# Kernel tuning notes

Measured on AMD Instinct MI355X. Metric: run time of the kernel, lower is better.

Reference implementation:

```python
import jax, jax.numpy as jnp
import numpy as np

N, T = 8, 64
V = [2048, 1024, 512, 256, 128]
E = [12288, 6144, 3072, 1536, 768]
NF = [1, 8, 16, 32, 64, 128]
LAT, INIT_DIM = 64, 16
K3 = 27  # 3x3x3 spline kernel bank


def setup_inputs():
    ks = iter(jax.random.split(jax.random.key(0), 80))
    inp = {}
    inp['x'] = jax.random.normal(next(ks), (N, V[0], T), jnp.float32)
    for l in range(5):
        inp['edge_index%d' % l] = jax.random.randint(next(ks), (2, E[l]), 0, V[l])
        inp['edge_attr%d' % l] = jax.random.uniform(next(ks), (E[l], 3), jnp.float32)
    pools = {'P01': (V[1], V[0]), 'P12': (V[2], V[1]), 'P23': (V[3], V[2]), 'P34': (V[4], V[3]),
             'P43': (V[3], V[4]), 'P32': (V[2], V[3]), 'P21': (V[1], V[2]), 'P10': (V[0], V[1])}
    for n, sh in pools.items():
        inp[n] = jax.random.normal(next(ks), sh, jnp.float32) / np.float32(np.sqrt(sh[1]))
    convs = {'conv1_w': (NF[0], NF[1]), 'conv2_w': (NF[1], NF[2]), 'conv3_w': (NF[2], NF[3]), 'conv4_w': (NF[3], NF[4]),
             'deconv4_w': (NF[4], NF[3]), 'deconv3_w': (NF[3], NF[2]), 'deconv2_w': (NF[2], NF[1]), 'deconv1_w': (NF[1], NF[0])}
    for n, (ci, co) in convs.items():
        inp[n] = jax.random.normal(next(ks), (K3, ci, co), jnp.float32) / np.float32(np.sqrt(ci * 8))
    def lin(k, o, i):
        return jax.random.normal(k, (o, i), jnp.float32) / np.float32(np.sqrt(i))
    inp['fce1_w'] = lin(next(ks), NF[5], NF[4]); inp['fce1_b'] = jnp.zeros((NF[5],), jnp.float32)
    inp['fce2_w'] = lin(next(ks), LAT, NF[5]); inp['fce2_b'] = jnp.zeros((LAT,), jnp.float32)
    inp['fcd3_w'] = lin(next(ks), NF[5], LAT); inp['fcd3_b'] = jnp.zeros((NF[5],), jnp.float32)
    inp['fcd4_w'] = lin(next(ks), NF[4], NF[5]); inp['fcd4_b'] = jnp.zeros((NF[4],), jnp.float32)
    for pre in ('dom', 'ini'):
        inp[pre + '_Wih'] = lin(next(ks), 3 * LAT, LAT)
        inp[pre + '_Whh'] = lin(next(ks), 3 * LAT, LAT)
        inp[pre + '_bih'] = jnp.zeros((3 * LAT,), jnp.float32)
        inp[pre + '_bhh'] = jnp.zeros((3 * LAT,), jnp.float32)
        inp[pre + '_agg_w'] = lin(next(ks), LAT, LAT)
        inp[pre + '_agg_b'] = jnp.zeros((LAT,), jnp.float32)
    for g in ('r', 'u', 'c'):
        inp['tr_W' + g] = lin(next(ks), LAT, 2 * LAT)
        inp['tr_b' + g] = jnp.zeros((LAT,), jnp.float32)
    return inp


def _edge_weights(attr, W):
    # Degree-1 B-spline basis over 3-dim pseudo-coords, kernel_size=3 per dim.
    pos = attr * 2.0                                    # [0, ks-1]
    i0 = jnp.clip(jnp.floor(pos), 0.0, 1.0).astype(jnp.int32)
    f = pos - i0                                        # fractional part
    We = jnp.zeros((attr.shape[0], W.shape[1], W.shape[2]), W.dtype)
    for c0 in (0, 1):
        w0 = f[:, 0] if c0 else 1.0 - f[:, 0]
        for c1 in (0, 1):
            w1 = f[:, 1] if c1 else 1.0 - f[:, 1]
            for c2 in (0, 1):
                w2 = f[:, 2] if c2 else 1.0 - f[:, 2]
                flat = (i0[:, 0] + c0) * 9 + (i0[:, 1] + c1) * 3 + (i0[:, 2] + c2)
                We = We + (w0 * w1 * w2)[:, None, None] * W[flat]
    return We                                           # (E, Ci, Co)


def _spatial_block(x, edge_index, edge_attr, W):
    # x: (N, V, Ci, T); edge-conditioned graph conv per time step, mean-aggregated, ELU.
    Nn, Vv, Ci, Tt = x.shape
    We = _edge_weights(edge_attr, W)                    # (E, Ci, Co)
    src, dst = edge_index[0], edge_index[1]
    msg = jnp.einsum('neit,eio->enot', x[:, src], We)   # (E, N, Co, T)
    agg = jax.ops.segment_sum(msg, dst, num_segments=Vv)
    deg = jax.ops.segment_sum(jnp.ones((dst.shape[0],), x.dtype), dst, num_segments=Vv)
    agg = agg / jnp.maximum(deg, 1.0)[:, None, None, None]
    return jax.nn.elu(agg.transpose(1, 0, 2, 3))        # (N, V, Co, T)


def _pw(x, Wl, b):
    # 1x1 Conv2d over channel dim: x (N, V, C, T)
    return jnp.einsum('nvct,oc->nvot', x, Wl) + b[None, None, :, None]


def _pool(h, P):
    # torch.matmul(P, x.view(N, V, C*T))
    Nn, Vv, Cc, Tt = h.shape
    return jnp.matmul(P, h.reshape(Nn, Vv, Cc * Tt)).reshape(Nn, P.shape[0], Cc, Tt)


def _rnn_encode(x, Wih, Whh, bih, bhh):
    # GRU over time per node; x (N, V, C, T) -> hidden seq (N, V, H, T)
    Nn, Vv, Cc, Tt = x.shape
    xt = x.transpose(3, 0, 1, 2).reshape(Tt, Nn * Vv, Cc)
    H = Whh.shape[1]
    def step(h, xi):
        gi = xi @ Wih.T + bih
        gh = h @ Whh.T + bhh
        ir, iz, ig = jnp.split(gi, 3, axis=-1)
        hr, hz, hg = jnp.split(gh, 3, axis=-1)
        r = jax.nn.sigmoid(ir + hr)
        z = jax.nn.sigmoid(iz + hz)
        g = jnp.tanh(ig + r * hg)
        hn = (1.0 - z) * g + z * h
        return hn, hn
    h0 = jnp.zeros((Nn * Vv, H), x.dtype)
    _, hs = jax.lax.scan(step, h0, xt)
    return hs.reshape(Tt, Nn, Vv, H).transpose(1, 2, 3, 0)


def reference(x, edge_attr0, edge_attr1, edge_attr2, edge_attr3, edge_attr4, P01, P12, P23, P34, P43, P32, P21, P10, conv1_w, conv2_w, conv3_w, conv4_w, deconv4_w, deconv3_w, deconv2_w, deconv1_w, fce1_w, fce1_b, fce2_w, fce2_b, fcd3_w, fcd3_b, fcd4_w, fcd4_b, dom_Wih, dom_Whh, dom_bih, dom_bhh, dom_agg_w, dom_agg_b, ini_Wih, ini_Whh, ini_bih, ini_bhh, ini_agg_w, ini_agg_b, tr_Wr, tr_br, tr_Wu, tr_bu, tr_Wc, tr_bc, edge_index0, edge_index1, edge_index2, edge_index3, edge_index4):
    h = x.reshape(N, V[0], NF[0], T)
    h = _pool(_spatial_block(h, edge_index0, edge_attr0, conv1_w), P01)
    h = _pool(_spatial_block(h, edge_index1, edge_attr1, conv2_w), P12)
    h = _pool(_spatial_block(h, edge_index2, edge_attr2, conv3_w), P23)
    h = _pool(_spatial_block(h, edge_index3, edge_attr3, conv4_w), P34)
    h = jax.nn.elu(_pw(h, fce1_w, fce1_b))
    embed = jnp.tanh(_pw(h, fce2_w, fce2_b))            # (N, V4, LAT, T)
    # ---- latent domain + initial state ----
    dom = _rnn_encode(embed, dom_Wih, dom_Whh, dom_bih, dom_bhh)
    z_D = jnp.tanh(dom[..., -1] @ dom_agg_w.T + dom_agg_b)
    ini = _rnn_encode(embed[..., :INIT_DIM], ini_Wih, ini_Whh, ini_bih, ini_bhh)
    z_0 = jnp.tanh(ini[..., -1] @ ini_agg_w.T + ini_agg_b)
    # ---- recurrent latent propagation over T steps (gated transition) ----
    def step(zp, _):
        cat = jnp.concatenate([zp, z_D], axis=-1)
        r = jax.nn.sigmoid(cat @ tr_Wr.T + tr_br)
        u = jax.nn.sigmoid(cat @ tr_Wu.T + tr_bu)
        c = jnp.tanh(jnp.concatenate([r * zp, z_D], axis=-1) @ tr_Wc.T + tr_bc)
        zt = (1.0 - u) * zp + u * c
        return zt, zt
    _, zs = jax.lax.scan(step, z_0, None, length=T)
    z = zs.transpose(1, 2, 3, 0)                        # (N, V4, LAT, T)
    h = jax.nn.elu(_pw(z, fcd3_w, fcd3_b))
    h = jax.nn.elu(_pw(h, fcd4_w, fcd4_b))
    h = _spatial_block(_pool(h, P43), edge_index3, edge_attr3, deconv4_w)
    h = _spatial_block(_pool(h, P32), edge_index2, edge_attr2, deconv3_w)
    h = _spatial_block(_pool(h, P21), edge_index1, edge_attr1, deconv2_w)
    h = _spatial_block(_pool(h, P10), edge_index0, edge_attr0, deconv1_w)
    return h.reshape(N, V[0], T)
```

## Files before the change

### kernel.cpp

```cpp
#include <hip/hip_runtime.h>

#define NB 8
#define TT 64

typedef __attribute__((ext_vector_type(8))) short bf16x8_t;
typedef __attribute__((ext_vector_type(4))) float f32x4_t;

__device__ __forceinline__ float sigm(float x){ return 1.0f/(1.0f+expf(-x)); }
__device__ __forceinline__ float eluf(float x){ return x>0.0f ? x : expm1f(x); }
__device__ __forceinline__ ushort f2bf(float f){
  uint u = __float_as_uint(f);
  return (ushort)((u + 0x7FFFu + ((u >> 16) & 1u)) >> 16);
}
__device__ __forceinline__ float bf2f(ushort u){
  return __uint_as_float(((uint)u) << 16);
}

__device__ __constant__ int c_VL[4] = {2048, 1024, 512, 256};
__device__ __constant__ int c_VO[4] = {0, 2048, 3072, 3584};
__device__ __constant__ int c_EO[4] = {0, 12288, 18432, 21504};
#define TOTV 3840
#define TOTE 23040

__global__ void transpose_kernel(const float* __restrict__ in, float* __restrict__ out, int R, int C){
  int idx = blockIdx.x*256 + threadIdx.x;
  if (idx >= R*C) return;
  int r = idx / C, c = idx - r*C;
  out[c*R + r] = in[idx];
}

__global__ void conv_bf16(const float* __restrict__ in, ushort* __restrict__ out, int n){
  int i = blockIdx.x*256 + threadIdx.x;
  if (i < n) out[i] = f2bf(in[i]);
}

__global__ void pad_wih(const float* __restrict__ in, ushort* __restrict__ out){
  int i = blockIdx.x*256 + threadIdx.x;
  if (i >= 256*64) return;
  int r = i >> 6;
  out[i] = (r < 192) ? f2bf(in[i]) : (ushort)0;
}

__global__ __launch_bounds__(256) void transp_bf16(
    const float* __restrict__ in, ushort* __restrict__ out, int R, int Ccols){
  __shared__ float tile[64][65];
  int n = blockIdx.z;
  const float* ip = in + (size_t)n*R*Ccols;
  ushort* op = out + (size_t)n*R*Ccols;
  int tid = threadIdx.x;
  int tx = tid & 63, ty = tid >> 6;
  int r0 = blockIdx.y*64, c0 = blockIdx.x*64;
  #pragma unroll
  for (int i = 0; i < 64; i += 4)
    tile[ty+i][tx] = ip[(size_t)(r0+ty+i)*Ccols + c0 + tx];
  __syncthreads();
  #pragma unroll
  for (int i = 0; i < 64; i += 4)
    op[(size_t)(c0+ty+i)*R + r0 + tx] = f2bf(tile[tx][ty+i]);
}

template<int Ci, int CiP>
__global__ __launch_bounds__(256) void xpose_bf16(const float* __restrict__ in, ushort* __restrict__ out){
  __shared__ float tile[Ci][65];
  int s = blockIdx.x, tid = threadIdx.x;
  const float* ip = in + (size_t)s*Ci*64;
  for (int i = tid; i < Ci*64; i += 256) tile[i>>6][i&63] = ip[i];
  __syncthreads();
  ushort* op = out + (size_t)s*64*CiP;
  for (int i = tid; i < 64*CiP; i += 256){
    int t = i / CiP, ci = i - t*CiP;
    op[i] = (ci < Ci) ? f2bf(tile[ci][t]) : (ushort)0;
  }
}

__global__ void csr_zero(int* __restrict__ deg_all){
  int i = blockIdx.x*256 + threadIdx.x;
  if (i < TOTV) deg_all[i] = 0;
}

__global__ void csr_deg(const int* __restrict__ d0, const int* __restrict__ d1,
                        const int* __restrict__ d2, const int* __restrict__ d3,
                        int* __restrict__ deg_all){
  int idx = blockIdx.x*256 + threadIdx.x;
  if (idx >= TOTE) return;
  int l = (idx < 12288) ? 0 : (idx < 18432) ? 1 : (idx < 21504) ? 2 : 3;
  int e = idx - c_EO[l];
  const int* dl = (l==0)?d0:(l==1)?d1:(l==2)?d2:d3;
  atomicAdd(&deg_all[c_VO[l] + dl[e]], 1);
}

__global__ __launch_bounds__(1024) void csr_scan(const int* __restrict__ deg_all,
                                                 int* __restrict__ rowptr_all,
                                                 int* __restrict__ cursor_all){
  __shared__ int a[2048], b[2048];
  int l = blockIdx.x;
  int Vv = c_VL[l], vo = c_VO[l], eo = c_EO[l];
  int tid = threadIdx.x;
  for (int i = tid; i < 2048; i += 1024) a[i] = (i < Vv) ? deg_all[vo + i] : 0;
  __syncthreads();
  int* s = a; int* d = b;
  for (int off = 1; off < 2048; off <<= 1){
    for (int i = tid; i < 2048; i += 1024) d[i] = s[i] + ((i >= off) ? s[i-off] : 0);
    __syncthreads();
    int* t = s; s = d; d = t;
  }
  int rbase = vo + l;
  for (int i = tid; i < Vv; i += 1024){
    int excl = (i == 0) ? 0 : s[i-1];
    rowptr_all[rbase + i] = excl;
    cursor_all[vo + i]    = eo + excl;
  }
  if (tid == 0) rowptr_all[rbase + Vv] = s[2047];
}

__global__ void csr_fill(const int* __restrict__ d0, const int* __restrict__ d1,
                         const int* __restrict__ d2, const int* __restrict__ d3,
                         int* __restrict__ cursor_all, int* __restrict__ elist_all){
  int idx = blockIdx.x*256 + threadIdx.x;
  if (idx >= TOTE) return;
  int l = (idx < 12288) ? 0 : (idx < 18432) ? 1 : (idx < 21504) ? 2 : 3;
  int e = idx - c_EO[l];
  const int* dl = (l==0)?d0:(l==1)?d1:(l==2)?d2:d3;
  int p = atomicAdd(&cursor_all[c_VO[l] + dl[e]], 1);
  elist_all[p] = e;
}

__global__ void csr_sort(const int* __restrict__ rowptr_all, int* __restrict__ elist_all){
  int idx = blockIdx.x*256 + threadIdx.x;
  if (idx >= TOTV) return;
  int l = (idx < 2048) ? 0 : (idx < 3072) ? 1 : (idx < 3584) ? 2 : 3;
  int v = idx - c_VO[l];
  int rbase = c_VO[l] + l, eo = c_EO[l];
  int s = eo + rowptr_all[rbase + v], epos = eo + rowptr_all[rbase + v + 1];
  for (int i = s + 1; i < epos; ++i){
    int key = elist_all[i];
    int j = i - 1;
    while (j >= s && elist_all[j] > key){ elist_all[j+1] = elist_all[j]; --j; }
    elist_all[j+1] = key;
  }
}

__global__ void edge_we_kernel(const float* __restrict__ attr, const float* __restrict__ Wb,
                               float* __restrict__ We, int E, int CiCo){
  int idx = blockIdx.x*256 + threadIdx.x;
  if (idx >= E*CiCo) return;
  int e = idx / CiCo, r = idx - e*CiCo;
  float f[3]; int i0[3];
  #pragma unroll
  for (int d = 0; d < 3; ++d){
    float p  = attr[e*3+d]*2.0f;
    float fl = fminf(fmaxf(floorf(p), 0.0f), 1.0f);
    i0[d] = (int)fl;
    f[d]  = p - fl;
  }
  float acc = 0.0f;
  #pragma unroll
  for (int c0 = 0; c0 < 2; ++c0){
    float w0 = c0 ? f[0] : 1.0f - f[0];
    #pragma unroll
    for (int c1 = 0; c1 < 2; ++c1){
      float w1 = c1 ? f[1] : 1.0f - f[1];
      #pragma unroll
      for (int c2 = 0; c2 < 2; ++c2){
        float w2 = c2 ? f[2] : 1.0f - f[2];
        int flat = (i0[0]+c0)*9 + (i0[1]+c1)*3 + (i0[2]+c2);
        acc += w0*w1*w2 * Wb[flat*CiCo + r];
      }
    }
  }
  We[idx] = acc;
}

template<int Ci, int Co, int CiP>
__global__ __launch_bounds__(256) void edge_weT2(
    const float* __restrict__ attr, const float* __restrict__ Wb,
    ushort* __restrict__ WeT){
  __shared__ float s[Ci][Co + 1];
  int e = blockIdx.x, tid = threadIdx.x;
  float f[3]; int i0[3];
  #pragma unroll
  for (int d = 0; d < 3; ++d){
    float p  = attr[e*3+d]*2.0f;
    float fl = fminf(fmaxf(floorf(p), 0.0f), 1.0f);
    i0[d] = (int)fl;
    f[d]  = p - fl;
  }
  float w[8]; int fl8[8];
  #pragma unroll
  for (int c0 = 0; c0 < 2; ++c0)
    #pragma unroll
    for (int c1 = 0; c1 < 2; ++c1)
      #pragma unroll
      for (int c2 = 0; c2 < 2; ++c2){
        int k = c0*4 + c1*2 + c2;
        w[k] = (c0 ? f[0] : 1.0f - f[0]) * (c1 ? f[1] : 1.0f - f[1]) * (c2 ? f[2] : 1.0f - f[2]);
        fl8[k] = (i0[0]+c0)*9 + (i0[1]+c1)*3 + (i0[2]+c2);
      }
  constexpr int CiCo = Ci*Co;
  for (int r = tid; r < CiCo; r += 256){
    float acc = 0.0f;
    #pragma unroll
    for (int k = 0; k < 8; ++k) acc += w[k]*Wb[fl8[k]*CiCo + r];
    s[r/Co][r - (r/Co)*Co] = acc;
  }
  __syncthreads();
  ushort* op = WeT + (size_t)e*(Co*CiP);
  for (int r2 = tid; r2 < Co*CiP; r2 += 256){
    int co = r2 / CiP, ci = r2 - co*CiP;
    op[r2] = (ci < Ci) ? f2bf(s[ci][co]) : (ushort)0;
  }
}

template<int Ci, int Co>
__global__ __launch_bounds__(256) void gconv2_kernel(
    const float* __restrict__ x, const float* __restrict__ We,
    const int* __restrict__ src_arr, const int* __restrict__ rowptr,
    const int* __restrict__ elist, float* __restrict__ out, int V){
  constexpr int CiCo = Ci*Co;
  __shared__ float ws[4][CiCo];
  __shared__ float red[Co*64];
  int blk = blockIdx.x;
  int n = blk / V, v = blk - n*V;
  int tid = threadIdx.x;
  int w = tid >> 6, lane = tid & 63;
  int rs = rowptr[v], re = rowptr[v+1];
  float acc[Co];
  #pragma unroll
  for (int i = 0; i < Co; ++i) acc[i] = 0.0f;

  for (int q = rs + w; q < re; q += 4){
    int e   = elist[q];
    int src = src_arr[e];
    const float* wsrc = We + (size_t)e*CiCo;
    #pragma unroll
    for (int i = lane; i < CiCo; i += 64) ws[w][i] = wsrc[i];
    __builtin_amdgcn_s_waitcnt(0);
    const float* xp = x + ((size_t)(n*V + src))*(Ci*64) + lane;
    #pragma unroll 4
    for (int ci = 0; ci < Ci; ++ci){
      float xv = xp[(size_t)ci*64];
      if constexpr (Co >= 4){
        #pragma unroll
        for (int co = 0; co < Co; co += 4){
          float4 wv = *(const float4*)&ws[w][ci*Co + co];
          acc[co+0] += wv.x*xv;
          acc[co+1] += wv.y*xv;
          acc[co+2] += wv.z*xv;
          acc[co+3] += wv.w*xv;
        }
      } else {
        #pragma unroll
        for (int co = 0; co < Co; ++co) acc[co] += ws[w][ci*Co + co]*xv;
      }
    }
  }

  if (w == 0){
    #pragma unroll
    for (int co = 0; co < Co; ++co) red[co*64 + lane] = acc[co];
  }
  __syncthreads();
  #pragma unroll
  for (int ww = 1; ww < 4; ++ww){
    if (w == ww){
      #pragma unroll
      for (int co = 0; co < Co; ++co) red[co*64 + lane] += acc[co];
    }
    __syncthreads();
  }
  float scale = 1.0f / fmaxf((float)(re - rs), 1.0f);
  size_t ob = ((size_t)(n*V + v))*(Co*64);
  for (int co = w; co < Co; co += 4)
    out[ob + (size_t)co*64 + lane] = eluf(red[co*64 + lane]*scale);
}

template<int CiP, int Co>
__global__ __launch_bounds__(256, 4) void gconv_mfma4(
    const ushort* __restrict__ xT, const ushort* __restrict__ WeT,
    const int* __restrict__ src_arr, const int* __restrict__ rowptr,
    const int* __restrict__ elist, float* __restrict__ out, int V){
  constexpr int MT = Co/16, KT = CiP/32;
  __shared__ int2 es[64];
  __shared__ float red[Co*64];
  int blk = blockIdx.x;
  int n = blk / V, v = blk - n*V;
  int tid = threadIdx.x;
  int w = tid >> 6, lane = tid & 63;
  int l15 = lane & 15, g = lane >> 4;
  int rs = rowptr[v], re = rowptr[v+1];
  int deg = re - rs;
  int cnt0 = (deg < 64) ? deg : 64;
  if (tid < cnt0){
    int e = elist[rs + tid];
    es[tid] = make_int2(e, src_arr[e]);
  }
  __syncthreads();
  f32x4_t acc[MT][4];
  #pragma unroll
  for (int m = 0; m < MT; ++m)
    #pragma unroll
    for (int tt = 0; tt < 4; ++tt) acc[m][tt] = (f32x4_t){0.f,0.f,0.f,0.f};
  for (int q = w; q < deg; q += 4){
    int e, src;
    if (q < 64){ e = es[q].x; src = es[q].y; }
    else { e = elist[rs + q]; src = src_arr[e]; }
    const ushort* xp = xT + ((size_t)(n*V + src))*(64*CiP) + (size_t)l15*CiP + g*8;
    const ushort* wp = WeT + (size_t)e*(Co*CiP) + (size_t)l15*CiP + g*8;
    #pragma unroll
    for (int kt = 0; kt < KT; ++kt){
      bf16x8_t bfrag[4];
      #pragma unroll
      for (int tt = 0; tt < 4; ++tt)
        bfrag[tt] = *(const bf16x8_t*)(xp + (size_t)tt*16*CiP + kt*32);
      #pragma unroll
      for (int m = 0; m < MT; ++m){
        bf16x8_t afrag = *(const bf16x8_t*)(wp + (size_t)m*16*CiP + kt*32);
        #pragma unroll
        for (int tt = 0; tt < 4; ++tt)
          acc[m][tt] = __builtin_amdgcn_mfma_f32_16x16x32_bf16(afrag, bfrag[tt], acc[m][tt], 0, 0, 0);
      }
    }
  }
  if (w == 0){
    #pragma unroll
    for (int m = 0; m < MT; ++m)
      #pragma unroll
      for (int tt = 0; tt < 4; ++tt)
        #pragma unroll
        for (int r = 0; r < 4; ++r)
          red[(m*16 + g*4 + r)*64 + tt*16 + l15] = acc[m][tt][r];
  }
  __syncthreads();
  #pragma unroll
  for (int ww = 1; ww < 4; ++ww){
    if (w == ww){
      #pragma unroll
      for (int m = 0; m < MT; ++m)
        #pragma unroll
        for (int tt = 0; tt < 4; ++tt)
          #pragma unroll
          for (int r = 0; r < 4; ++r)
            red[(m*16 + g*4 + r)*64 + tt*16 + l15] += acc[m][tt][r];
    }
    __syncthreads();
  }
  float scale = 1.0f / fmaxf((float)deg, 1.0f);
  size_t ob = ((size_t)(n*V + v))*(Co*64);
  for (int i = tid; i < Co*64; i += 256)
    out[ob + i] = eluf(red[i]*scale);
}

template<int OUTBF>
__global__ __launch_bounds__(256) void pool_mfma64(
    const ushort* __restrict__ A, const ushort* __restrict__ BT, void* __restrict__ Cout,
    int M, int K, int NN){
  __shared__ ushort As[64*40];
  __shared__ ushort Bs[64*40];
  char* Asb = (char*)As; char* Bsb = (char*)Bs;
  int tid = threadIdx.x;
  int wv = tid >> 6, lane = tid & 63;
  int g = lane >> 4, l15 = lane & 15;
  int wr = wv >> 1, wc = wv & 1;
  int m0 = blockIdx.y*64, n0 = blockIdx.x*64;
  const ushort* Bp = BT + (size_t)blockIdx.z*((size_t)NN*K);
  f32x4_t acc[2][2];
  #pragma unroll
  for (int i = 0; i < 2; ++i)
    #pragma unroll
    for (int j = 0; j < 2; ++j) acc[i][j] = (f32x4_t){0.f,0.f,0.f,0.f};
  int srow = tid >> 2, slot = tid & 3;
  int wbo = srow*80 + slot*16;
  const ushort* gA = A  + (size_t)(m0+srow)*K + slot*8;
  const ushort* gB = Bp + (size_t)(n0+srow)*K + slot*8;
  for (int k0 = 0; k0 < K; k0 += 32){
    uint4 va = *(const uint4*)(gA + k0);
    uint4 vb = *(const uint4*)(gB + k0);
    __syncthreads();
    *(uint4*)(Asb + wbo) = va;
    *(uint4*)(Bsb + wbo) = vb;
    __syncthreads();
    bf16x8_t af[2], bfr[2];
    #pragma unroll
    for (int f = 0; f < 2; ++f){
      af[f]  = *(const bf16x8_t*)(Asb + (wr*32 + f*16 + l15)*80 + g*16);
      bfr[f] = *(const bf16x8_t*)(Bsb + (wc*32 + f*16 + l15)*80 + g*16);
    }
    #pragma unroll
    for (int fm = 0; fm < 2; ++fm)
      #pragma unroll
      for (int fn = 0; fn < 2; ++fn)
        acc[fm][fn] = __builtin_amdgcn_mfma_f32_16x16x32_bf16(af[fm], bfr[fn], acc[fm][fn], 0, 0, 0);
  }
  #pragma unroll
  for (int fm = 0; fm < 2; ++fm){
    int row = m0 + wr*32 + fm*16 + g*4;
    #pragma unroll
    for (int fn = 0; fn < 2; ++fn){
      int col = n0 + wc*32 + fn*16 + l15;
      if constexpr (OUTBF){
        ushort* Cb = (ushort*)Cout + (size_t)blockIdx.z*((size_t)M*NN);
        #pragma unroll
        for (int r = 0; r < 4; ++r)
          Cb[(size_t)(row + r)*NN + col] = f2bf(acc[fm][fn][r]);
      } else {
        float* Cf = (float*)Cout + (size_t)blockIdx.z*((size_t)M*NN);
        #pragma unroll
        for (int r = 0; r < 4; ++r)
          Cf[(size_t)(row + r)*NN + col] = acc[fm][fn][r];
      }
    }
  }
}

template<int C, int O1, int O2, int ACT1, int ACT2, int INF, int OUTF>
__global__ __launch_bounds__(256) void pw2_mfma(
    const void* __restrict__ inv,
    const ushort* __restrict__ W1, const float* __restrict__ b1,
    const ushort* __restrict__ W2, const float* __restrict__ b2,
    void* __restrict__ outv){
  constexpr int CP = C + 8, O1P = O1 + 8;
  constexpr int MT1 = O1/16, KT1 = C/32;
  constexpr int MT2 = O2/16, KT2 = O1/32;
  __shared__ ushort XT[64*CP];
  __shared__ ushort YT[64*O1P];
  int s = blockIdx.x, tid = threadIdx.x;
  int w = tid >> 6, lane = tid & 63;
  int l15 = lane & 15, g = lane >> 4;
  if constexpr (INF == 0){
    const float* ip = (const float*)inv + (size_t)s*C*64;
    for (int i = tid; i < C*64; i += 256){ int c = i >> 6, t = i & 63; XT[t*CP + c] = f2bf(ip[i]); }
  } else {
    const float* ip = (const float*)inv + (size_t)s*64*C;
    for (int i = tid; i < C*64; i += 256){ int t = i / C, c = i - t*C; XT[t*CP + c] = f2bf(ip[i]); }
  }
  __syncthreads();
  int trow = w*16 + l15;
  {
    f32x4_t acc[MT1];
    #pragma unroll
    for (int m = 0; m < MT1; ++m) acc[m] = (f32x4_t){0.f,0.f,0.f,0.f};
    #pragma unroll
    for (int kt = 0; kt < KT1; ++kt){
      bf16x8_t bfrag = *(const bf16x8_t*)(&XT[trow*CP + kt*32 + g*8]);
      #pragma unroll
      for (int m = 0; m < MT1; ++m){
        bf16x8_t afrag = *(const bf16x8_t*)(W1 + (size_t)(m*16 + l15)*C + kt*32 + g*8);
        acc[m] = __builtin_amdgcn_mfma_f32_16x16x32_bf16(afrag, bfrag, acc[m], 0, 0, 0);
      }
    }
    #pragma unroll
    for (int m = 0; m < MT1; ++m){
      #pragma unroll
      for (int r = 0; r < 4; ++r){
        int o = m*16 + g*4 + r;
        float v = acc[m][r] + b1[o];
        v = (ACT1 == 1) ? eluf(v) : tanhf(v);
        YT[trow*O1P + o] = f2bf(v);
      }
    }
  }
  __syncthreads();
  {
    f32x4_t acc[MT2];
    #pragma unroll
    for (int m = 0; m < MT2; ++m) acc[m] = (f32x4_t){0.f,0.f,0.f,0.f};
    #pragma unroll
    for (int kt = 0; kt < KT2; ++kt){
      bf16x8_t bfrag = *(const bf16x8_t*)(&YT[trow*O1P + kt*32 + g*8]);
      #pragma unroll
      for (int m = 0; m < MT2; ++m){
        bf16x8_t afrag = *(const bf16x8_t*)(W2 + (size_t)(m*16 + l15)*O1 + kt*32 + g*8);
        acc[m] = __builtin_amdgcn_mfma_f32_16x16x32_bf16(afrag, bfrag, acc[m], 0, 0, 0);
      }
    }
    if constexpr (OUTF == 0){
      float* op = (float*)outv + (size_t)s*O2*64;
      #pragma unroll
      for (int m = 0; m < MT2; ++m){
        #pragma unroll
        for (int r = 0; r < 4; ++r){
          int o = m*16 + g*4 + r;
          float v = acc[m][r] + b2[o];
          v = (ACT2 == 1) ? eluf(v) : tanhf(v);
          op[(size_t)o*64 + trow] = v;
        }
      }
    } else {
      constexpr int O2P = O2 + 8;
      #pragma unroll
      for (int m = 0; m < MT2; ++m){
        #pragma unroll
        for (int r = 0; r < 4; ++r){
          int o = m*16 + g*4 + r;
          float v = acc[m][r] + b2[o];
          v = (ACT2 == 1) ? eluf(v) : tanhf(v);
          XT[trow*O2P + o] = f2bf(v);
        }
      }
      __syncthreads();
      ushort* op = (ushort*)outv + (size_t)s*64*O2;
      for (int i = tid; i < 64*O2; i += 256){
        int t = i / O2, o = i - t*O2;
        op[i] = XT[t*O2P + o];
      }
    }
  }
}

__global__ __launch_bounds__(192) void gru3m_kernel(
    const ushort* __restrict__ GI_d, const ushort* __restrict__ GI_i,
    const float* __restrict__ WhhT_d, const float* __restrict__ WhhT_i,
    const float* __restrict__ bih_d, const float* __restrict__ bhh_d,
    const float* __restrict__ aggT_d, const float* __restrict__ aggb_d,
    const float* __restrict__ bih_i, const float* __restrict__ bhh_i,
    const float* __restrict__ aggT_i, const float* __restrict__ aggb_i,
    float* __restrict__ zD, float* __restrict__ z0, int S){
  __shared__ float hsh[64];
  __shared__ float rbuf[64];
  __shared__ float zbuf[64];
  int bid = blockIdx.x;
  bool dom = (bid < S);
  int s = dom ? bid : bid - S;
  int TS = dom ? 64 : 16;
  const ushort* GI   = dom ? GI_d   : GI_i;
  const float* WhhT  = dom ? WhhT_d : WhhT_i;
  const float* bih   = dom ? bih_d  : bih_i;
  const float* bhh   = dom ? bhh_d  : bhh_i;
  const float* aggT  = dom ? aggT_d : aggT_i;
  const float* aggb  = dom ? aggb_d : aggb_i;
  float* zout        = dom ? zD     : z0;
  int tid = threadIdx.x;
  int g = tid >> 6, j = tid & 63;
  if (tid < 64) hsh[tid] = 0.0f;
  float whh[64];
  #pragma unroll
  for (int c = 0; c < 64; ++c) whh[c] = WhhT[c*192 + tid];
  float b_i = bih[tid], b_h = bhh[tid];
  const ushort* gp = GI + (size_t)s*64*256 + tid;
  float gi_cur = b_i + bf2f(gp[0]);
  __syncthreads();
  for (int t = 0; t < TS; ++t){
    ushort gnx = (t + 1 < TS) ? gp[(size_t)(t+1)*256] : (ushort)0;
    float gh0 = 0.f, gh1 = 0.f;
    #pragma unroll
    for (int c4 = 0; c4 < 16; ++c4){
      float4 hv = *(const float4*)&hsh[c4*4];
      gh0 += whh[c4*4+0]*hv.x; gh1 += whh[c4*4+1]*hv.y;
      gh0 += whh[c4*4+2]*hv.z; gh1 += whh[c4*4+3]*hv.w;
    }
    float gh = b_h + gh0 + gh1;
    if (g == 0)      rbuf[j] = sigm(gi_cur + gh);
    else if (g == 1) zbuf[j] = sigm(gi_cur + gh);
    __syncthreads();
    if (g == 2){
      float gg = tanhf(gi_cur + rbuf[j]*gh);
      float z  = zbuf[j];
      hsh[j] = (1.0f - z)*gg + z*hsh[j];
    }
    __syncthreads();
    gi_cur = b_i + bf2f(gnx);
  }
  if (tid < 64){
    float a = aggb[tid];
    #pragma unroll
    for (int c = 0; c < 64; ++c) a += aggT[c*64 + tid]*hsh[c];
    zout[(size_t)s*64 + tid] = tanhf(a);
  }
}

__global__ __launch_bounds__(192) void trans2_kernel(
    const float* __restrict__ z0, const float* __restrict__ zD,
    const float* __restrict__ WrT, const float* __restrict__ WuT, const float* __restrict__ WcT,
    const float* __restrict__ br, const float* __restrict__ bu, const float* __restrict__ bc,
    float* __restrict__ zs){
  __shared__ float zp[64];
  __shared__ float zd[64];
  __shared__ float rz[64];
  __shared__ float ubuf[64];
  int s = blockIdx.x, tid = threadIdx.x;
  int g = tid >> 6, j = tid & 63;
  if (tid < 64){ zp[tid] = z0[(size_t)s*64 + tid]; zd[tid] = zD[(size_t)s*64 + tid]; }
  const float* WT = (g == 0) ? WrT : (g == 1) ? WuT : WcT;
  const float* bb = (g == 0) ? br  : (g == 1) ? bu  : bc;
  float wv[64];
  #pragma unroll
  for (int c = 0; c < 64; ++c) wv[c] = WT[c*64 + j];
  float bconst = bb[j];
  __syncthreads();
  {
    float a0 = 0.f, a1 = 0.f;
    #pragma unroll
    for (int c4 = 0; c4 < 16; ++c4){
      float4 dv = *(const float4*)&zd[c4*4];
      a0 += WT[(64 + c4*4 + 0)*64 + j]*dv.x;
      a1 += WT[(64 + c4*4 + 1)*64 + j]*dv.y;
      a0 += WT[(64 + c4*4 + 2)*64 + j]*dv.z;
      a1 += WT[(64 + c4*4 + 3)*64 + j]*dv.w;
    }
    bconst += a0 + a1;
  }
  for (int t = 0; t < 64; ++t){
    if (g < 2){
      float a0 = 0.f, a1 = 0.f;
      #pragma unroll
      for (int c4 = 0; c4 < 16; ++c4){
        float4 pv = *(const float4*)&zp[c4*4];
        a0 += wv[c4*4+0]*pv.x; a1 += wv[c4*4+1]*pv.y;
        a0 += wv[c4*4+2]*pv.z; a1 += wv[c4*4+3]*pv.w;
      }
      float v = sigm(bconst + a0 + a1);
      if (g == 0) rz[j]   = v*zp[j];
      else        ubuf[j] = v;
    }
    __syncthreads();
    if (g == 2){
      float a0 = 0.f, a1 = 0.f;
      #pragma unroll
      for (int c4 = 0; c4 < 16; ++c4){
        float4 rv = *(const float4*)&rz[c4*4];
        a0 += wv[c4*4+0]*rv.x; a1 += wv[c4*4+1]*rv.y;
        a0 += wv[c4*4+2]*rv.z; a1 += wv[c4*4+3]*rv.w;
      }
      float cc = tanhf(bconst + a0 + a1);
      float u  = ubuf[j];
      float zt = (1.0f - u)*zp[j] + u*cc;
      zs[(size_t)s*4096 + t*64 + j] = zt;
      zp[j] = zt;
    }
    __syncthreads();
  }
}

extern "C" void kernel_launch(void* const* d_in, const int* in_sizes, int n_in,
                              void* d_out, int out_size, void* d_ws, size_t ws_size,
                              hipStream_t stream){
  static const int Vl[5] = {2048, 1024, 512, 256, 128};
  static const int El[5] = {12288, 6144, 3072, 1536, 768};
  static const int VO[4] = {0, 2048, 3072, 3584};
  static const int EO[4] = {0, 12288, 18432, 21504};

  const float* xin = (const float*)d_in[0];
  const int*   ei[4]; const float* ea[4];
  for (int l = 0; l < 4; ++l){ ei[l] = (const int*)d_in[1 + 2*l]; ea[l] = (const float*)d_in[2 + 2*l]; }
  const float* Psrc[8] = {(const float*)d_in[11], (const float*)d_in[12], (const float*)d_in[13], (const float*)d_in[14],
                          (const float*)d_in[15], (const float*)d_in[16], (const float*)d_in[17], (const float*)d_in[18]};
  const float* conv_w[4]   = {(const float*)d_in[19], (const float*)d_in[20], (const float*)d_in[21], (const float*)d_in[22]};
  const float* deconv_w[4] = {(const float*)d_in[23], (const float*)d_in[24], (const float*)d_in[25], (const float*)d_in[26]};
  const float* fce1_w = (const float*)d_in[27]; const float* fce1_b = (const float*)d_in[28];
  const float* fce2_w = (const float*)d_in[29]; const float* fce2_b = (const float*)d_in[30];
  const float* fcd3_w = (const float*)d_in[31]; const float* fcd3_b = (const float*)d_in[32];
  const float* fcd4_w = (const float*)d_in[33]; const float* fcd4_b = (const float*)d_in[34];
  const float* dom_Wih = (const float*)d_in[35]; const float* dom_Whh = (const float*)d_in[36];
  const float* dom_bih = (const float*)d_in[37]; const float* dom_bhh = (const float*)d_in[38];
  const float* dom_aggw = (const float*)d_in[39]; const float* dom_aggb = (const float*)d_in[40];
  const float* ini_Wih = (const float*)d_in[41]; const float* ini_Whh = (const float*)d_in[42];
  const float* ini_bih = (const float*)d_in[43]; const float* ini_bhh = (const float*)d_in[44];
  const float* ini_aggw = (const float*)d_in[45]; const float* ini_aggb = (const float*)d_in[46];
  const float* tr_Wr = (const float*)d_in[47]; const float* tr_br = (const float*)d_in[48];
  const float* tr_Wu = (const float*)d_in[49]; const float* tr_bu = (const float*)d_in[50];
  const float* tr_Wc = (const float*)d_in[51]; const float* tr_bc = (const float*)d_in[52];

  char* wsp = (char*)d_ws;
  size_t off = 0;
  auto carve = [&](size_t bytes) -> void* {
    void* p = wsp + off;
    off = (off + bytes + 255) & ~(size_t)255;
    return p;
  };
  const size_t BUFCAP = (size_t)NB*2048*8*64;
  float* bufA = (float*)carve(BUFCAP*4);
  float* bufB = (float*)carve(BUFCAP*4);
  void* webt = carve((size_t)NB*1024*1024*2 + 1024);
  float*  We = (float*)webt;
  ushort* BT = (ushort*)webt;
  ushort* xT = (ushort*)webt;
  ushort* WeTb = (ushort*)carve((size_t)1536*64*32*2 + 1024);
  ushort* embB2 = (ushort*)carve((size_t)1024*64*64*2);
  float* zD   = (float*)carve((size_t)NB*128*64*4);
  float* z0   = (float*)carve((size_t)NB*128*64*4);
  float* domWhhT = (float*)carve(12288*4);
  float* iniWhhT = (float*)carve(12288*4);
  float* domAggT = (float*)carve(4096*4);
  float* iniAggT = (float*)carve(4096*4);
  float* trWrT   = (float*)carve(8192*4);
  float* trWuT   = (float*)carve(8192*4);
  float* trWcT   = (float*)carve(8192*4);
  ushort* WihPadD = (ushort*)carve(256*64*2);
  ushort* WihPadI = (ushort*)carve(256*64*2);
  ushort* Wfce1b = (ushort*)carve(8192*2);
  ushort* Wfce2b = (ushort*)carve(8192*2);
  ushort* Wfcd3b = (ushort*)carve(8192*2);
  ushort* Wfcd4b = (ushort*)carve(8192*2);
  static const int PM[8] = {1024, 512, 256, 128, 256, 512, 1024, 2048};
  static const int PK[8] = {2048, 1024, 512, 256, 128, 256, 512, 1024};
  ushort* Pb[8];
  for (int i = 0; i < 8; ++i) Pb[i] = (ushort*)carve((size_t)PM[i]*PK[i]*2);
  int* deg_all    = (int*)carve(TOTV*4);
  int* cursor_all = (int*)carve(TOTV*4);
  int* rowptr_all = (int*)carve((TOTV + 4)*4);
  int* elist_all  = (int*)carve(TOTE*4);
  (void)ws_size; (void)in_sizes; (void)n_in; (void)out_size;

  auto tr = [&](const float* in, float* out, int R, int C){
    transpose_kernel<<<(R*C + 255)/256, 256, 0, stream>>>(in, out, R, C);
  };
  tr(dom_Whh, domWhhT, 192, 64);  tr(ini_Whh, iniWhhT, 192, 64);
  tr(dom_aggw, domAggT, 64, 64);  tr(ini_aggw, iniAggT, 64, 64);
  tr(tr_Wr, trWrT, 64, 128);  tr(tr_Wu, trWuT, 64, 128);  tr(tr_Wc, trWcT, 64, 128);
  pad_wih<<<64, 256, 0, stream>>>(dom_Wih, WihPadD);
  pad_wih<<<64, 256, 0, stream>>>(ini_Wih, WihPadI);
  conv_bf16<<<32, 256, 0, stream>>>(fce1_w, Wfce1b, 8192);
  conv_bf16<<<32, 256, 0, stream>>>(fce2_w, Wfce2b, 8192);
  conv_bf16<<<32, 256, 0, stream>>>(fcd3_w, Wfcd3b, 8192);
  conv_bf16<<<32, 256, 0, stream>>>(fcd4_w, Wfcd4b, 8192);
  for (int i = 0; i < 8; ++i){
    int nel = PM[i]*PK[i];
    conv_bf16<<<(nel + 255)/256, 256, 0, stream>>>(Psrc[i], Pb[i], nel);
  }

  const int* dsts[4] = {ei[0] + El[0], ei[1] + El[1], ei[2] + El[2], ei[3] + El[3]};
  csr_zero<<<(TOTV + 255)/256, 256, 0, stream>>>(deg_all);
  csr_deg <<<(TOTE + 255)/256, 256, 0, stream>>>(dsts[0], dsts[1], dsts[2], dsts[3], deg_all);
  csr_scan<<<4, 1024, 0, stream>>>(deg_all, rowptr_all, cursor_all);
  csr_fill<<<(TOTE + 255)/256, 256, 0, stream>>>(dsts[0], dsts[1], dsts[2], dsts[3], cursor_all, elist_all);
  csr_sort<<<(TOTV + 255)/256, 256, 0, stream>>>(rowptr_all, elist_all);

  auto gconv = [&](const float* in, float* out, int l, const float* Wb, int Ci, int Co){
    int CiCo = Ci*Co;
    int tot = El[l]*CiCo;
    edge_we_kernel<<<(tot + 255)/256, 256, 0, stream>>>(ea[l], Wb, We, El[l], CiCo);
    int nblk = NB*Vl[l];
    const int* rp = rowptr_all + VO[l] + l;
    const int* el = elist_all + EO[l];
    #define GCASE(CI,CO) if (Ci==CI && Co==CO) gconv2_kernel<CI,CO><<<nblk, 256, 0, stream>>>(in, We, ei[l], rp, el, out, Vl[l]);
    GCASE(1,8)  GCASE(8,16)  GCASE(16,8)  GCASE(8,1)
    #undef GCASE
  };
  auto gconv_m = [&](const float* in, float* out, int l, const float* Wb, int Ci, int Co){
    int S = NB*Vl[l];
    int CiP = (Ci < 32) ? 32 : Ci;
    if (Ci == 16)      xpose_bf16<16,32><<<S, 256, 0, stream>>>(in, xT);
    else if (Ci == 32) xpose_bf16<32,32><<<S, 256, 0, stream>>>(in, xT);
    else               xpose_bf16<64,64><<<S, 256, 0, stream>>>(in, xT);
    if (Ci == 16 && Co == 32)      edge_weT2<16,32,32><<<El[l], 256, 0, stream>>>(ea[l], Wb, WeTb);
    else if (Ci == 32 && Co == 64) edge_weT2<32,64,32><<<El[l], 256, 0, stream>>>(ea[l], Wb, WeTb);
    else if (Ci == 64 && Co == 32) edge_weT2<64,32,64><<<El[l], 256, 0, stream>>>(ea[l], Wb, WeTb);
    else if (Ci == 32 && Co == 16) edge_weT2<32,16,32><<<El[l], 256, 0, stream>>>(ea[l], Wb, WeTb);
    const int* rp = rowptr_all + VO[l] + l;
    const int* el = elist_all + EO[l];
    #define GMC(CIP,CO) if (CiP==CIP && Co==CO) gconv_mfma4<CIP,CO><<<S, 256, 0, stream>>>(xT, WeTb, ei[l], rp, el, out, Vl[l]);
    GMC(32,32) GMC(32,64) GMC(64,32) GMC(32,16)
    #undef GMC
  };
  auto pool2 = [&](int pi, const float* hin, float* out, int M, int K, int NN){
    dim3 tg(NN/64, K/64, NB);
    transp_bf16<<<tg, 256, 0, stream>>>(hin, BT, K, NN);
    dim3 g(NN/64, M/64, NB);
    pool_mfma64<0><<<g, 256, 0, stream>>>(Pb[pi], BT, (void*)out, M, K, NN);
  };

  gconv(xin,  bufA, 0, conv_w[0], 1, 8);
  pool2(0, bufA, bufB, 1024, 2048, 512);
  gconv(bufB, bufA, 1, conv_w[1], 8, 16);
  pool2(1, bufA, bufB, 512, 1024, 1024);
  gconv_m(bufB, bufA, 2, conv_w[2], 16, 32);
  pool2(2, bufA, bufB, 256, 512, 2048);
  gconv_m(bufB, bufA, 3, conv_w[3], 32, 64);
  pool2(3, bufA, bufB, 128, 256, 4096);

  pw2_mfma<64,128,64,1,2,0,1><<<1024, 256, 0, stream>>>(bufB, Wfce1b, fce1_b, Wfce2b, fce2_b, embB2);

  dim3 gg(4, 1024, 1);
  pool_mfma64<1><<<gg, 256, 0, stream>>>(embB2, WihPadD, (void*)bufA, 65536, 64, 256);
  pool_mfma64<1><<<gg, 256, 0, stream>>>(embB2, WihPadI, (void*)bufB, 65536, 64, 256);
  gru3m_kernel<<<2*NB*128, 192, 0, stream>>>((const ushort*)bufA, (const ushort*)bufB,
      domWhhT, iniWhhT, dom_bih, dom_bhh, domAggT, dom_aggb,
      ini_bih, ini_bhh, iniAggT, ini_aggb, zD, z0, NB*128);
  trans2_kernel<<<NB*128, 192, 0, stream>>>(z0, zD, trWrT, trWuT, trWcT, tr_br, tr_bu, tr_bc, bufA);

  pw2_mfma<64,128,64,1,1,1,0><<<1024, 256, 0, stream>>>(bufA, Wfcd3b, fcd3_b, Wfcd4b, fcd4_b, bufB);
  pool2(4, bufB, bufA, 256, 128, 4096);
  gconv_m(bufA, bufB, 3, deconv_w[0], 64, 32);
  pool2(5, bufB, bufA, 512, 256, 2048);
  gconv_m(bufA, bufB, 2, deconv_w[1], 32, 16);
  pool2(6, bufB, bufA, 1024, 512, 1024);
  gconv(bufA, bufB, 1, deconv_w[2], 16, 8);
  pool2(7, bufB, bufA, 2048, 1024, 512);
  gconv(bufA, (float*)d_out, 0, deconv_w[3], 8, 1);
}
```

Measured before the change: 808.9 us.

## Batch weight-prep launches, merge input-gate GEMMs, and reorder gconv block mapping

Replaces about twenty small weight transpose and bf16-conversion launches with a single task-table kernel, which cuts launch overhead. The two GRU input-projection GEMMs become one GEMM against a concatenated 512-wide weight, and the GRU kernel reads the interleaved output with a 512 stride. The MFMA graph-conv kernel also remaps block IDs so consecutive blocks cover all batches of a node group, aiming for better cache reuse of shared edge weights. The remap assumes V is a multiple of 8 and NB equals 8.

```diff
diff --git a/kernel.cpp b/kernel.cpp
--- a/kernel.cpp
+++ b/kernel.cpp
@@ -22,23 +22,34 @@
 #define TOTV 3840
 #define TOTE 23040
 
-__global__ void transpose_kernel(const float* __restrict__ in, float* __restrict__ out, int R, int C){
-  int idx = blockIdx.x*256 + threadIdx.x;
-  if (idx >= R*C) return;
-  int r = idx / C, c = idx - r*C;
-  out[c*R + r] = in[idx];
-}
-
-__global__ void conv_bf16(const float* __restrict__ in, ushort* __restrict__ out, int n){
-  int i = blockIdx.x*256 + threadIdx.x;
-  if (i < n) out[i] = f2bf(in[i]);
-}
-
-__global__ void pad_wih(const float* __restrict__ in, ushort* __restrict__ out){
-  int i = blockIdx.x*256 + threadIdx.x;
-  if (i >= 256*64) return;
-  int r = i >> 6;
-  out[i] = (r < 192) ? f2bf(in[i]) : (ushort)0;
+#define NPREP 21
+struct PrepTasks {
+  const float* src[NPREP];
+  void* dst[NPREP];
+  int R[NPREP], C[NPREP];
+  int type[NPREP];
+  int blk0[NPREP + 1];
+  int ntask;
+};
+
+__global__ __launch_bounds__(256) void prep_all(PrepTasks T){
+  int b = blockIdx.x;
+  int t = 0;
+  while (t + 1 < T.ntask && b >= T.blk0[t+1]) ++t;
+  int idx = (b - T.blk0[t])*256 + threadIdx.x;
+  int n = T.R[t]*T.C[t];
+  if (idx >= n) return;
+  int ty = T.type[t];
+  if (ty == 0){
+    int C = T.C[t];
+    int r = idx / C, c = idx - r*C;
+    ((float*)T.dst[t])[c*T.R[t] + r] = T.src[t][idx];
+  } else if (ty == 1){
+    int r = idx >> 6;
+    ((ushort*)T.dst[t])[idx] = (r < 192) ? f2bf(T.src[t][idx]) : (ushort)0;
+  } else {
+    ((ushort*)T.dst[t])[idx] = f2bf(T.src[t][idx]);
+  }
 }
 
 __global__ __launch_bounds__(256) void transp_bf16(
@@ -282,8 +293,10 @@
   constexpr int MT = Co/16, KT = CiP/32;
   __shared__ int2 es[64];
   __shared__ float red[Co*64];
-  int blk = blockIdx.x;
-  int n = blk / V, v = blk - n*V;
+  int bid = blockIdx.x;
+  int r8 = bid & 7, q0 = bid >> 3;
+  int n = q0 & 7;
+  int v = ((q0 >> 3) << 3) | r8;
   int tid = threadIdx.x;
   int w = tid >> 6, lane = tid & 63;
   int l15 = lane & 15, g = lane >> 4;
@@ -508,7 +521,7 @@
 }
 
 __global__ __launch_bounds__(192) void gru3m_kernel(
-    const ushort* __restrict__ GI_d, const ushort* __restrict__ GI_i,
+    const ushort* __restrict__ GI,
     const float* __restrict__ WhhT_d, const float* __restrict__ WhhT_i,
     const float* __restrict__ bih_d, const float* __restrict__ bhh_d,
     const float* __restrict__ aggT_d, const float* __restrict__ aggb_d,
@@ -522,7 +535,6 @@
   bool dom = (bid < S);
   int s = dom ? bid : bid - S;
   int TS = dom ? 64 : 16;
-  const ushort* GI   = dom ? GI_d   : GI_i;
   const float* WhhT  = dom ? WhhT_d : WhhT_i;
   const float* bih   = dom ? bih_d  : bih_i;
   const float* bhh   = dom ? bhh_d  : bhh_i;
@@ -536,11 +548,11 @@
   #pragma unroll
   for (int c = 0; c < 64; ++c) whh[c] = WhhT[c*192 + tid];
   float b_i = bih[tid], b_h = bhh[tid];
-  const ushort* gp = GI + (size_t)s*64*256 + tid;
+  const ushort* gp = GI + (size_t)s*64*512 + (dom ? 0 : 256) + tid;
   float gi_cur = b_i + bf2f(gp[0]);
   __syncthreads();
   for (int t = 0; t < TS; ++t){
-    ushort gnx = (t + 1 < TS) ? gp[(size_t)(t+1)*256] : (ushort)0;
+    ushort gnx = (t + 1 < TS) ? gp[(size_t)(t+1)*512] : (ushort)0;
     float gh0 = 0.f, gh1 = 0.f;
     #pragma unroll
     for (int c4 = 0; c4 < 16; ++c4){
@@ -685,8 +697,7 @@
   float* trWrT   = (float*)carve(8192*4);
   float* trWuT   = (float*)carve(8192*4);
   float* trWcT   = (float*)carve(8192*4);
-  ushort* WihPadD = (ushort*)carve(256*64*2);
-  ushort* WihPadI = (ushort*)carve(256*64*2);
+  ushort* WihPad2 = (ushort*)carve(512*64*2);
   ushort* Wfce1b = (ushort*)carve(8192*2);
   ushort* Wfce2b = (ushort*)carve(8192*2);
   ushort* Wfcd3b = (ushort*)carve(8192*2);
@@ -701,22 +712,29 @@
   int* elist_all  = (int*)carve(TOTE*4);
   (void)ws_size; (void)in_sizes; (void)n_in; (void)out_size;
 
-  auto tr = [&](const float* in, float* out, int R, int C){
-    transpose_kernel<<<(R*C + 255)/256, 256, 0, stream>>>(in, out, R, C);
+  PrepTasks T;
+  int nt = 0;
+  auto addT = [&](const float* s, void* d, int R, int C, int ty){
+    T.src[nt] = s; T.dst[nt] = d; T.R[nt] = R; T.C[nt] = C; T.type[nt] = ty; ++nt;
   };
-  tr(dom_Whh, domWhhT, 192, 64);  tr(ini_Whh, iniWhhT, 192, 64);
-  tr(dom_aggw, domAggT, 64, 64);  tr(ini_aggw, iniAggT, 64, 64);
-  tr(tr_Wr, trWrT, 64, 128);  tr(tr_Wu, trWuT, 64, 128);  tr(tr_Wc, trWcT, 64, 128);
-  pad_wih<<<64, 256, 0, stream>>>(dom_Wih, WihPadD);
-  pad_wih<<<64, 256, 0, stream>>>(ini_Wih, WihPadI);
-  conv_bf16<<<32, 256, 0, stream>>>(fce1_w, Wfce1b, 8192);
-  conv_bf16<<<32, 256, 0, stream>>>(fce2_w, Wfce2b, 8192);
-  conv_bf16<<<32, 256, 0, stream>>>(fcd3_w, Wfcd3b, 8192);
-  conv_bf16<<<32, 256, 0, stream>>>(fcd4_w, Wfcd4b, 8192);
-  for (int i = 0; i < 8; ++i){
-    int nel = PM[i]*PK[i];
-    conv_bf16<<<(nel + 255)/256, 256, 0, stream>>>(Psrc[i], Pb[i], nel);
-  }
+  addT(dom_Whh, domWhhT, 192, 64, 0);
+  addT(ini_Whh, iniWhhT, 192, 64, 0);
+  addT(dom_aggw, domAggT, 64, 64, 0);
+  addT(ini_aggw, iniAggT, 64, 64, 0);
+  addT(tr_Wr, trWrT, 64, 128, 0);
+  addT(tr_Wu, trWuT, 64, 128, 0);
+  addT(tr_Wc, trWcT, 64, 128, 0);
+  addT(dom_Wih, WihPad2, 256, 64, 1);
+  addT(ini_Wih, WihPad2 + 256*64, 256, 64, 1);
+  addT(fce1_w, Wfce1b, 128, 64, 2);
+  addT(fce2_w, Wfce2b, 64, 128, 2);
+  addT(fcd3_w, Wfcd3b, 128, 64, 2);
+  addT(fcd4_w, Wfcd4b, 64, 128, 2);
+  for (int i = 0; i < 8; ++i) addT(Psrc[i], Pb[i], PM[i], PK[i], 2);
+  T.ntask = nt;
+  T.blk0[0] = 0;
+  for (int i = 0; i < nt; ++i) T.blk0[i+1] = T.blk0[i] + (T.R[i]*T.C[i] + 255)/256;
+  prep_all<<<T.blk0[nt], 256, 0, stream>>>(T);
 
   const int* dsts[4] = {ei[0] + El[0], ei[1] + El[1], ei[2] + El[2], ei[3] + El[3]};
   csr_zero<<<(TOTV + 255)/256, 256, 0, stream>>>(deg_all);
@@ -770,10 +788,9 @@
 
   pw2_mfma<64,128,64,1,2,0,1><<<1024, 256, 0, stream>>>(bufB, Wfce1b, fce1_b, Wfce2b, fce2_b, embB2);
 
-  dim3 gg(4, 1024, 1);
-  pool_mfma64<1><<<gg, 256, 0, stream>>>(embB2, WihPadD, (void*)bufA, 65536, 64, 256);
-  pool_mfma64<1><<<gg, 256, 0, stream>>>(embB2, WihPadI, (void*)bufB, 65536, 64, 256);
-  gru3m_kernel<<<2*NB*128, 192, 0, stream>>>((const ushort*)bufA, (const ushort*)bufB,
+  dim3 gg(8, 1024, 1);
+  pool_mfma64<1><<<gg, 256, 0, stream>>>(embB2, WihPad2, (void*)bufA, 65536, 64, 512);
+  gru3m_kernel<<<2*NB*128, 192, 0, stream>>>((const ushort*)bufA,
       domWhhT, iniWhhT, dom_bih, dom_bhh, domAggT, dom_aggb,
       ini_bih, ini_bhh, iniAggT, ini_aggb, zD, z0, NB*128);
   trans2_kernel<<<NB*128, 192, 0, stream>>>(z0, zD, trWrT, trWuT, trWcT, tr_br, tr_bu, tr_bc, bufA);
```

Result: faster. 791.4 us (-2.2%).
